# Performance work log

Measured on AMD Instinct MI355X. Metric: run time of the kernel, lower is better.

Reference implementation:

```python
import jax, jax.numpy as jnp
import numpy as np

B, C, H, W, CI, COUT = 4, 256, 48, 48, 128, 1024


def conv1x1(x, w, b):
    # 1x1 conv: x (b,c,h,w), w (o,c), b (o,)
    return jnp.einsum('bchw,oc->bohw', x, w) + b[None, :, None, None]


def setup_inputs() -> dict:
    key = jax.random.key(0)
    ks = jax.random.split(key, 24)
    s = 0.05
    d = {
        'x': jax.random.normal(ks[0], (B, C, H, W), jnp.float32),
        'x1': jax.random.normal(ks[1], (B, C, H, W), jnp.float32),
        'x2': jax.random.normal(ks[2], (B, C, H, W), jnp.float32),
        'x_in': jax.random.normal(ks[3], (B, COUT, H, W), jnp.float32),
        'g_w': jax.random.normal(ks[4], (CI, C), jnp.float32) * s,
        'g_b': jnp.zeros((CI,), jnp.float32),
        'th_w': jax.random.normal(ks[5], (CI, C), jnp.float32) * s,
        'th_b': jnp.zeros((CI,), jnp.float32),
        'ph_w': jax.random.normal(ks[6], (CI, C), jnp.float32) * s,
        'ph_b': jnp.zeros((CI,), jnp.float32),
        'th1_w': jax.random.normal(ks[7], (CI, C), jnp.float32) * s,
        'th1_b': jnp.zeros((CI,), jnp.float32),
        'ph1_w': jax.random.normal(ks[8], (CI, C), jnp.float32) * s,
        'ph1_b': jnp.zeros((CI,), jnp.float32),
        'th2_w': jax.random.normal(ks[9], (CI, C), jnp.float32) * s,
        'th2_b': jnp.zeros((CI,), jnp.float32),
        'ph2_w': jax.random.normal(ks[10], (CI, C), jnp.float32) * s,
        'ph2_b': jnp.zeros((CI,), jnp.float32),
        'W_w': jax.random.normal(ks[11], (C, CI), jnp.float32) * s,
        'W_b': jnp.zeros((C,), jnp.float32),
        'W1_w': jax.random.normal(ks[12], (C, CI), jnp.float32) * s,
        'W1_b': jnp.zeros((C,), jnp.float32),
        'W2_w': jax.random.normal(ks[13], (C, CI), jnp.float32) * s,
        'W2_b': jnp.zeros((C,), jnp.float32),
        'dw_w': jax.random.normal(ks[14], (3 * C,), jnp.float32) * s,   # depthwise 1x1 = per-channel scale
        'dw_b': jnp.zeros((3 * C,), jnp.float32),
        'pw_w': jax.random.normal(ks[15], (COUT, 3 * C), jnp.float32) * s,
        'pw_b': jnp.zeros((COUT,), jnp.float32),
        'p': jnp.array([0.5], jnp.float32),
    }
    return d


def reference(x, x1, x2, x_in, g_w, g_b, th_w, th_b, ph_w, ph_b,
              th1_w, th1_b, ph1_w, ph1_b, th2_w, th2_b, ph2_w, ph2_b,
              W_w, W_b, W1_w, W1_b, W2_w, W2_b, dw_w, dw_b, pw_w, pw_b, p):
    b, _, h, w = x.shape
    n = h * w

    def flat(v):  # (b,c,h,w) -> (b,c,n)
        return v.reshape(b, v.shape[1], n)

    # g projections (same g applied to x, x1, x2); MaxPool(1) is identity
    g_x = flat(conv1x1(x, g_w, g_b)).transpose(0, 2, 1)    # (b,n,ci)
    g_x1 = flat(conv1x1(x1, g_w, g_b)).transpose(0, 2, 1)
    g_x2 = flat(conv1x1(x2, g_w, g_b)).transpose(0, 2, 1)

    # three attention branches (unscaled QK^T softmax)
    def attn(v, tw, tb, pw, pb):
        theta = flat(conv1x1(v, tw, tb)).transpose(0, 2, 1)  # (b,n,ci)
        phi = flat(conv1x1(v, pw, pb))                       # (b,ci,n)
        f = jnp.einsum('bnc,bcm->bnm', theta, phi)           # (b,n,n)
        return jax.nn.softmax(f, axis=-1)

    A = attn(x, th_w, th_b, ph_w, ph_b)
    A = A + attn(x1, th1_w, th1_b, ph1_w, ph1_b)
    A = A + attn(x2, th2_w, th2_b, ph2_w, ph2_b)  # sum of the three softmax maps

    def mix(gv, Ww, Wb, res):
        # y = (A0+A1+A2) @ g  ==  A0@g + A1@g + A2@g (distributive, exact)
        y = jnp.einsum('bnm,bmc->bnc', A, gv)                # (b,n,ci)
        y = y.transpose(0, 2, 1).reshape(b, CI, h, w)
        return conv1x1(y, Ww, Wb) + res

    z = mix(g_x, W_w, W_b, x)
    z1 = mix(g_x1, W1_w, W1_b, x1)
    z2 = mix(g_x2, W2_w, W2_b, x2)

    cat = jnp.concatenate([z, z1, z2], axis=1)               # (b,768,h,w)
    # DWConv: depthwise 1x1 (per-channel scale+bias) then pointwise 1x1
    dw = cat * dw_w[None, :, None, None] + dw_b[None, :, None, None]
    out = conv1x1(dw, pw_w, pw_b)                            # (b,1024,h,w)
    return x_in + p[0] * out
```

## Files before the change

kernel.cpp:

```cpp
#include <hip/hip_runtime.h>


typedef __attribute__((ext_vector_type(8))) short bf16x8;
typedef __attribute__((ext_vector_type(4))) float f32x4;
typedef unsigned short u16;
struct alignas(8) u16x4 { u16 x, y, z, w; };
struct alignas(16) u16x8 { u16 e[8]; };

constexpr int B_ = 4, C_ = 256, N_ = 2304, CI_ = 128;
constexpr long long NN_ = (long long)N_ * N_;

constexpr size_t B_WB = 0;
constexpr size_t B_WZ = 589824;
constexpr size_t B_PW = 786432;
constexpr size_t B_R1 = 2359296;
constexpr size_t B_R2 = 16515072;
constexpr size_t B_GP = 30670848;
constexpr size_t B_F  = 37748736;
constexpr size_t B_A  = 69599232;

__device__ __forceinline__ u16 f2bf(float f) {
  unsigned u = __float_as_uint(f);
  u += 0x7fff + ((u >> 16) & 1);
  return (u16)(u >> 16);
}
__device__ __forceinline__ u16 f2h(float f) {
  _Float16 h = (_Float16)f;
  return __builtin_bit_cast(u16, h);
}
__device__ __forceinline__ float h2f(u16 u) {
  return (float)__builtin_bit_cast(_Float16, u);
}

__device__ __forceinline__ void gload16(const void* g, void* l) {
  __builtin_amdgcn_global_load_lds((const __attribute__((address_space(1))) void*)g,
                                   (__attribute__((address_space(3))) void*)l,
                                   16, 0, 0);
}

template<int N> __device__ __forceinline__ void vwait() {
  asm volatile("s_waitcnt vmcnt(%0)" :: "i"(N) : "memory");
}
__device__ __forceinline__ void barrier_() {
  asm volatile("" ::: "memory");
  __builtin_amdgcn_s_barrier();
  asm volatile("" ::: "memory");
}

__device__ __forceinline__ int xcd_swz() {
  const int nwg = (int)gridDim.x, orig = (int)blockIdx.x;
  const int q = nwg >> 3, r = nwg & 7;
  const int xcd = orig & 7, pos = orig >> 3;
  return (xcd < r ? xcd * (q + 1) : r * (q + 1) + (xcd - r) * q) + pos;
}

__device__ __forceinline__ void stage32(const char* Ag, int ldaB,
                                        const char* Bg, int ldbB,
                                        char* As, char* Bs, int t) {
  #pragma unroll
  for (int c = 0; c < 2; ++c) {
    const int idx = (c * 256 + t) * 16;
    const int row = idx >> 6;
    const int gc = (idx & 63) ^ (((row >> 1) & 3) << 4);
    gload16(Ag + (size_t)row * ldaB + gc, As + idx);
    gload16(Bg + (size_t)row * ldbB + gc, Bs + idx);
  }
}

__device__ __forceinline__ void comp32(const char* As, const char* Bs,
                                       f32x4 (&acc)[4][4],
                                       int arow, int brow, int kb) {
  bf16x8 af[4], bfr[4];
  #pragma unroll
  for (int i = 0; i < 4; ++i) {
    af[i]  = *(const bf16x8*)(As + (arow + i * 16) * 64 + kb);
    bfr[i] = *(const bf16x8*)(Bs + (brow + i * 16) * 64 + kb);
  }
  __builtin_amdgcn_s_setprio(1);
  #pragma unroll
  for (int mf = 0; mf < 4; ++mf)
    #pragma unroll
    for (int nf = 0; nf < 4; ++nf)
      acc[mf][nf] = __builtin_amdgcn_mfma_f32_16x16x32_bf16(
          af[mf], bfr[nf], acc[mf][nf], 0, 0, 0);
  __builtin_amdgcn_s_setprio(0);
}

__device__ __forceinline__ void gemm256c(const char* Ab, int ldaB,
                                         const char* Bb, int ldbB,
                                         int kIters, f32x4 (&acc)[4][4],
                                         char* lds) {
  const int t = (int)threadIdx.x, l = t & 63, w = t >> 6;
  const int arow = (w >> 1) * 64 + (l & 15);
  const int brow = (w & 1) * 64 + (l & 15);
  const int kb = ((l >> 4) * 16) ^ ((((l & 15) >> 1) & 3) << 4);
  char* A0 = lds;          char* B0 = lds + 8192;
  char* A1 = lds + 16384;  char* B1 = lds + 24576;
  char* A2 = lds + 32768;  char* B2 = lds + 40960;
  stage32(Ab,      ldaB, Bb,      ldbB, A0, B0, t);
  stage32(Ab + 64, ldaB, Bb + 64, ldbB, A1, B1, t);
  for (int kt = 0; kt < kIters - 2; ++kt) {
    stage32(Ab + (size_t)(kt + 2) * 64, ldaB,
            Bb + (size_t)(kt + 2) * 64, ldbB, A2, B2, t);
    vwait<8>();
    barrier_();
    comp32(A0, B0, acc, arow, brow, kb);
    barrier_();
    char* ta = A0; A0 = A1; A1 = A2; A2 = ta;
    char* tb = B0; B0 = B1; B1 = B2; B2 = tb;
  }
  vwait<4>();
  barrier_();
  comp32(A0, B0, acc, arow, brow, kb);
  vwait<0>();
  barrier_();
  comp32(A1, B1, acc, arow, brow, kb);
}

#define EPI_SETUP \
  const int el = (int)threadIdx.x & 63, ew = (int)threadIdx.x >> 6; \
  const int rb = (ew >> 1) * 64 + ((el >> 4) << 2); \
  const int cb = (ew & 1) * 64 + (el & 15);

struct CvtW { const float* s[13]; };
__global__ __launch_bounds__(256) void k_cvtw(CvtW cw, u16* dst) {
  const int seg = blockIdx.y;
  const int i = (blockIdx.x * 256 + threadIdx.x) * 4;
  const int sz = (seg == 12) ? 786432 : 32768;
  if (i >= sz) return;
  size_t off = (seg < 9) ? (size_t)seg * 32768
             : (seg < 12) ? 294912 + (size_t)(seg - 9) * 32768
                          : 393216;
  f32x4 v = *(const f32x4*)(cw.s[seg] + i);
  u16x4 o; o.x = f2bf(v[0]); o.y = f2bf(v[1]); o.z = f2bf(v[2]); o.w = f2bf(v[3]);
  *(u16x4*)(dst + off + i) = o;
}

__global__ __launch_bounds__(256) void k_cvtx(const float* x0, const float* x1,
                                              const float* x2, u16* XT) {
  __shared__ float tile[64][65];
  const int t = threadIdx.x;
  const int q0 = blockIdx.x * 64, c0 = blockIdx.y * 64;
  const int vb = blockIdx.z, v = vb >> 2, b = vb & 3;
  const float* src = (v == 0 ? x0 : v == 1 ? x1 : x2) + ((size_t)b * C_ + c0) * N_ + q0;
  #pragma unroll
  for (int i = 0; i < 4; ++i) {
    int idx = t + i * 256;
    int r = idx >> 4, q4 = (idx & 15) * 4;
    f32x4 val = *(const f32x4*)(src + (size_t)r * N_ + q4);
    tile[r][q4 + 0] = val[0]; tile[r][q4 + 1] = val[1];
    tile[r][q4 + 2] = val[2]; tile[r][q4 + 3] = val[3];
  }
  __syncthreads();
  u16* dst = XT + ((size_t)vb * N_ + q0) * 256 + c0;
  const int q = t >> 2, cp = (t & 3) * 16;
  u16 tmp[16];
  #pragma unroll
  for (int jj = 0; jj < 16; ++jj) tmp[jj] = f2bf(tile[cp + jj][q]);
  #pragma unroll
  for (int s4 = 0; s4 < 4; ++s4) {
    u16x4 o; o.x = tmp[s4 * 4]; o.y = tmp[s4 * 4 + 1];
    o.z = tmp[s4 * 4 + 2]; o.w = tmp[s4 * 4 + 3];
    *(u16x4*)(dst + (size_t)q * 256 + cp + s4 * 4) = o;
  }
}

struct ProjA { const float* bias[9]; };
__global__ __launch_bounds__(256) void k_proj(const u16* WB, const u16* XT,
                                              u16* TH, u16* PH, u16* GP, ProjA pa) {
  __shared__ char lds[49152];
  const int col0 = blockIdx.x * 128;
  const int p = blockIdx.z >> 2, b = blockIdx.z & 3;
  const int v = p / 3, pt = p % 3;
  const char* Ab = (const char*)(WB + (size_t)p * 32768);
  const char* Bb = (const char*)(XT + ((size_t)(v * 4 + b) * N_ + col0) * 256);
  f32x4 acc[4][4] = {};
  gemm256c(Ab, 512, Bb, 512, 8, acc, lds);
  EPI_SETUP;
  const float* bias = pa.bias[p];
  if (pt == 0) {
    u16* dst = GP + (size_t)(v * 4 + b) * CI_ * N_;
    #pragma unroll
    for (int mf = 0; mf < 4; ++mf) {
      const int row = rb + mf * 16;
      f32x4 bv = *(const f32x4*)(bias + row);
      #pragma unroll
      for (int nf = 0; nf < 4; ++nf) {
        const int col = col0 + cb + nf * 16;
        #pragma unroll
        for (int r = 0; r < 4; ++r)
          dst[(size_t)(row + r) * N_ + col] = f2bf(acc[mf][nf][r] + bv[r]);
      }
    }
  } else {
    u16* dst = (pt == 1 ? TH : PH) + (size_t)(v * 4 + b) * N_ * CI_;
    #pragma unroll
    for (int mf = 0; mf < 4; ++mf) {
      const int row = rb + mf * 16;
      f32x4 bv = *(const f32x4*)(bias + row);
      #pragma unroll
      for (int nf = 0; nf < 4; ++nf) {
        const int col = col0 + cb + nf * 16;
        u16x4 o;
        o.x = f2bf(acc[mf][nf][0] + bv[0]); o.y = f2bf(acc[mf][nf][1] + bv[1]);
        o.z = f2bf(acc[mf][nf][2] + bv[2]); o.w = f2bf(acc[mf][nf][3] + bv[3]);
        *(u16x4*)(dst + (size_t)col * CI_ + row) = o;
      }
    }
  }
}

__global__ __launch_bounds__(256) void k_score(const u16* TH, const u16* PH,
                                               u16* F, int b) {
  __shared__ char lds[49152];
  const int col0 = blockIdx.x * 128;
  const int row0 = blockIdx.y * 128;
  const int br = blockIdx.z;
  const char* Ab = (const char*)(TH + ((size_t)(br * 4 + b) * N_ + row0) * CI_);
  const char* Bb = (const char*)(PH + ((size_t)(br * 4 + b) * N_ + col0) * CI_);
  f32x4 acc[4][4] = {};
  gemm256c(Ab, 256, Bb, 256, 4, acc, lds);
  EPI_SETUP;
  const int t = (int)threadIdx.x;
  __syncthreads();
  u16* tl = (u16*)lds;
  #pragma unroll
  for (int mf = 0; mf < 4; ++mf)
    #pragma unroll
    for (int nf = 0; nf < 4; ++nf)
      #pragma unroll
      for (int r = 0; r < 4; ++r)
        tl[(rb + mf * 16 + r) * 136 + cb + nf * 16] = f2h(acc[mf][nf][r]);
  __syncthreads();
  u16* dst = F + (size_t)br * NN_;
  const int k8 = (t & 15) * 8;
  #pragma unroll
  for (int rr = 0; rr < 8; ++rr) {
    const int q = (t >> 4) + rr * 16;
    *(u16x8*)(dst + (size_t)(row0 + q) * N_ + col0 + k8) =
        *(const u16x8*)(tl + q * 136 + k8);
  }
}

__device__ __forceinline__ float blk_sum(float v, float* red) {
  #pragma unroll
  for (int o = 32; o; o >>= 1) v += __shfl_xor(v, o);
  int w = threadIdx.x >> 6;
  __syncthreads();
  if ((threadIdx.x & 63) == 0) red[w] = v;
  __syncthreads();
  return red[0] + red[1] + red[2] + red[3];
}

__global__ __launch_bounds__(256) void k_softsum(const u16* F, u16* Abf, int b) {
  __shared__ float red[4];
  const int q = blockIdx.x, t = threadIdx.x;
  const bool ext = (t < 32);
  float outv[16] = {};
  #pragma unroll
  for (int i = 0; i < 3; ++i) {
    const u16* base = F + (size_t)i * NN_ + (size_t)q * N_;
    float e[16];
    u16x8 a = *(const u16x8*)(base + t * 8);
    #pragma unroll
    for (int jj = 0; jj < 8; ++jj) e[jj] = __expf(h2f(a.e[jj]));
    if (ext) {
      u16x8 c = *(const u16x8*)(base + 2048 + t * 8);
      #pragma unroll
      for (int jj = 0; jj < 8; ++jj) e[8 + jj] = __expf(h2f(c.e[jj]));
    } else {
      #pragma unroll
      for (int jj = 0; jj < 8; ++jj) e[8 + jj] = 0.f;
    }
    float ssum = 0.f;
    #pragma unroll
    for (int s = 0; s < 16; ++s) ssum += e[s];
    ssum = blk_sum(ssum, red);
    const float inv = 1.f / ssum;
    #pragma unroll
    for (int s = 0; s < 16; ++s) outv[s] += e[s] * inv;
  }
  u16* dst = Abf + ((size_t)b * N_ + q) * N_;
  u16x8 o;
  #pragma unroll
  for (int jj = 0; jj < 8; ++jj) o.e[jj] = f2bf(outv[jj]);
  *(u16x8*)(dst + t * 8) = o;
  if (ext) {
    #pragma unroll
    for (int jj = 0; jj < 8; ++jj) o.e[jj] = f2bf(outv[8 + jj]);
    *(u16x8*)(dst + 2048 + t * 8) = o;
  }
}

__global__ __launch_bounds__(256) void k_pv(const u16* Abf, const u16* GP,
                                            float* P) {
  __shared__ char lds[49152];
  const int lid = xcd_swz();
  const int j = lid % 3;
  const int row0 = ((lid / 3) % 18) * 128;
  const int z = lid / 54;
  const int b = z >> 1, s = z & 1;
  const char* Ab = (const char*)(Abf + ((size_t)b * N_ + row0) * N_ + s * 1152);
  const char* Bb = (const char*)(GP + (size_t)(j * 4 + b) * CI_ * N_ + s * 1152);
  f32x4 acc[4][4] = {};
  gemm256c(Ab, 4608, Bb, 4608, 36, acc, lds);
  EPI_SETUP;
  const int t = (int)threadIdx.x;
  float* dst = P + ((size_t)(s * 4 + b) * N_) * 384;
  float* tl = (float*)lds;
  const int jc4 = (t & 15) * 4;
  #pragma unroll
  for (int p = 0; p < 2; ++p) {
    __syncthreads();
    if ((ew & 1) == p) {
      #pragma unroll
      for (int mf = 0; mf < 4; ++mf)
        #pragma unroll
        for (int nf = 0; nf < 4; ++nf)
          #pragma unroll
          for (int r = 0; r < 4; ++r)
            tl[(rb + mf * 16 + r) * 68 + (el & 15) + nf * 16] = acc[mf][nf][r];
    }
    __syncthreads();
    #pragma unroll
    for (int rr = 0; rr < 8; ++rr) {
      const int q = (t >> 4) + rr * 16;
      *(f32x4*)(dst + (size_t)(row0 + q) * 384 + j * 128 + p * 64 + jc4) =
          *(const f32x4*)(tl + q * 68 + jc4);
    }
  }
}

__global__ __launch_bounds__(256) void k_pvred(const float* P, u16* Y) {
  const size_t i4 = (size_t)blockIdx.x * 256 + threadIdx.x;
  constexpr size_t HALF = (size_t)4 * N_ * 384;
  f32x4 a = *(const f32x4*)(P + i4 * 4);
  f32x4 c = *(const f32x4*)(P + HALF + i4 * 4);
  u16x4 o; o.x = f2bf(a[0] + c[0]); o.y = f2bf(a[1] + c[1]);
  o.z = f2bf(a[2] + c[2]); o.w = f2bf(a[3] + c[3]);
  *(u16x4*)(Y + i4 * 4) = o;
}

struct ZA { const float* x[3]; const float* wzb[3]; const float* dww; const float* dwb; };
__global__ __launch_bounds__(256) void k_zcat(const u16* WZ, const u16* Y,
                                              u16* DW, ZA za) {
  __shared__ char lds[49152];
  const int col0 = blockIdx.x * 128;
  const int row0 = blockIdx.y * 128;
  const int j = blockIdx.z >> 2, b = blockIdx.z & 3;
  const char* Ab = (const char*)(WZ + (size_t)j * 32768 + (size_t)row0 * CI_);
  const char* Bb = (const char*)(Y + ((size_t)b * N_ + col0) * 384 + j * CI_);
  f32x4 acc[4][4] = {};
  gemm256c(Ab, 256, Bb, 768, 4, acc, lds);
  EPI_SETUP;
  const float* xj = za.x[j];
  #pragma unroll
  for (int mf = 0; mf < 4; ++mf) {
    const int cl = row0 + rb + mf * 16;
    const int cg = j * 256 + cl;
    f32x4 wb = *(const f32x4*)(za.wzb[j] + cl);
    f32x4 sc = *(const f32x4*)(za.dww + cg);
    f32x4 sb = *(const f32x4*)(za.dwb + cg);
    #pragma unroll
    for (int nf = 0; nf < 4; ++nf) {
      const int qg = col0 + cb + nf * 16;
      u16x4 o;
      o.x = f2bf((acc[mf][nf][0] + wb[0] + xj[((size_t)b * C_ + cl + 0) * N_ + qg]) * sc[0] + sb[0]);
      o.y = f2bf((acc[mf][nf][1] + wb[1] + xj[((size_t)b * C_ + cl + 1) * N_ + qg]) * sc[1] + sb[1]);
      o.z = f2bf((acc[mf][nf][2] + wb[2] + xj[((size_t)b * C_ + cl + 2) * N_ + qg]) * sc[2] + sb[2]);
      o.w = f2bf((acc[mf][nf][3] + wb[3] + xj[((size_t)b * C_ + cl + 3) * N_ + qg]) * sc[3] + sb[3]);
      *(u16x4*)(DW + ((size_t)b * N_ + qg) * 768 + cg) = o;
    }
  }
}

__global__ __launch_bounds__(256) void k_final(const u16* PWb, const u16* DW,
                                               const float* pwb, const float* xin,
                                               const float* pp, float* out) {
  __shared__ char lds[49152];
  const int lid = xcd_swz();
  const int row0 = (lid % 18) * 128;
  const int col0 = ((lid / 18) % 8) * 128;
  const int b = lid / 144;
  const char* Ab = (const char*)(DW + ((size_t)b * N_ + row0) * 768);
  const char* Bb = (const char*)(PWb + (size_t)col0 * 768);
  EPI_SETUP;
  const int t = (int)threadIdx.x;
  const float pscale = pp[0];
  const int q4 = (t & 31) * 4;
  const int ob = (t >> 5) * 8;
  f32x4 xv[2][8];
  #pragma unroll
  for (int p = 0; p < 2; ++p)
    #pragma unroll
    for (int rr = 0; rr < 8; ++rr)
      xv[p][rr] = *(const f32x4*)(
          xin + ((size_t)b * 1024 + col0 + p * 64 + ob + rr) * N_ + row0 + q4);
  f32x4 acc[4][4] = {};
  gemm256c(Ab, 1536, Bb, 1536, 24, acc, lds);
  float* tl = (float*)lds;
  #pragma unroll
  for (int p = 0; p < 2; ++p) {
    __syncthreads();
    if ((ew & 1) == p) {
      #pragma unroll
      for (int mf = 0; mf < 4; ++mf)
        #pragma unroll
        for (int nf = 0; nf < 4; ++nf)
          #pragma unroll
          for (int r = 0; r < 4; ++r)
            tl[((el & 15) + nf * 16) * 132 + rb + mf * 16 + r] = acc[mf][nf][r];
    }
    __syncthreads();
    #pragma unroll
    for (int rr = 0; rr < 8; ++rr) {
      const int og = col0 + p * 64 + ob + rr;
      const float bb = pwb[og];
      f32x4 a4 = *(const f32x4*)(tl + (ob + rr) * 132 + q4);
      f32x4 o4;
      #pragma unroll
      for (int r = 0; r < 4; ++r)
        o4[r] = xv[p][rr][r] + pscale * (a4[r] + bb);
      *(f32x4*)(out + ((size_t)b * 1024 + og) * N_ + row0 + q4) = o4;
    }
  }
}

extern "C" void kernel_launch(void* const* d_in, const int* in_sizes, int n_in,
                              void* d_out, int out_size, void* d_ws, size_t ws_size,
                              hipStream_t stream) {
  const float* x0  = (const float*)d_in[0];
  const float* x1  = (const float*)d_in[1];
  const float* x2  = (const float*)d_in[2];
  const float* xin = (const float*)d_in[3];
  const float* g_w = (const float*)d_in[4];
  const float* g_b = (const float*)d_in[5];
  const float* thw[3] = {(const float*)d_in[6],  (const float*)d_in[10], (const float*)d_in[14]};
  const float* thb[3] = {(const float*)d_in[7],  (const float*)d_in[11], (const float*)d_in[15]};
  const float* phw[3] = {(const float*)d_in[8],  (const float*)d_in[12], (const float*)d_in[16]};
  const float* phb[3] = {(const float*)d_in[9],  (const float*)d_in[13], (const float*)d_in[17]};
  const float* Wm[3]  = {(const float*)d_in[18], (const float*)d_in[20], (const float*)d_in[22]};
  const float* Wmb[3] = {(const float*)d_in[19], (const float*)d_in[21], (const float*)d_in[23]};
  const float* dww = (const float*)d_in[24];
  const float* dwb = (const float*)d_in[25];
  const float* pww = (const float*)d_in[26];
  const float* pwb = (const float*)d_in[27];
  const float* pp  = (const float*)d_in[28];

  char* wsb = (char*)d_ws;
  u16*   WB  = (u16*)(wsb + B_WB);
  u16*   WZ  = (u16*)(wsb + B_WZ);
  u16*   PW  = (u16*)(wsb + B_PW);
  u16*   XT  = (u16*)(wsb + B_R1);
  u16*   Y   = (u16*)(wsb + B_R1);
  u16*   TH  = (u16*)(wsb + B_R2);
  u16*   PH  = TH + (size_t)3 * B_ * N_ * CI_;
  u16*   DW  = (u16*)(wsb + B_R2);
  u16*   GP  = (u16*)(wsb + B_GP);
  u16*   Fh  = (u16*)(wsb + B_F);
  float* Pp  = (float*)(wsb + B_F);
  u16*   Abf = (u16*)(wsb + B_A);

  CvtW cw;
  cw.s[0] = g_w; cw.s[1] = thw[0]; cw.s[2] = phw[0];
  cw.s[3] = g_w; cw.s[4] = thw[1]; cw.s[5] = phw[1];
  cw.s[6] = g_w; cw.s[7] = thw[2]; cw.s[8] = phw[2];
  cw.s[9] = Wm[0]; cw.s[10] = Wm[1]; cw.s[11] = Wm[2];
  cw.s[12] = pww;

  ProjA pa;
  pa.bias[0] = g_b; pa.bias[1] = thb[0]; pa.bias[2] = phb[0];
  pa.bias[3] = g_b; pa.bias[4] = thb[1]; pa.bias[5] = phb[1];
  pa.bias[6] = g_b; pa.bias[7] = thb[2]; pa.bias[8] = phb[2];

  ZA za;
  za.x[0] = x0; za.x[1] = x1; za.x[2] = x2;
  za.wzb[0] = Wmb[0]; za.wzb[1] = Wmb[1]; za.wzb[2] = Wmb[2];
  za.dww = dww; za.dwb = dwb;

  k_cvtw<<<dim3(768, 13), 256, 0, stream>>>(cw, WB);
  k_cvtx<<<dim3(36, 4, 12), 256, 0, stream>>>(x0, x1, x2, XT);
  k_proj<<<dim3(18, 1, 36), 256, 0, stream>>>(WB, XT, TH, PH, GP, pa);
  for (int b = 0; b < B_; ++b) {
    k_score  <<<dim3(18, 18, 3), 256, 0, stream>>>(TH, PH, Fh, b);
    k_softsum<<<dim3(N_),        256, 0, stream>>>(Fh, Abf, b);
  }
  k_pv   <<<dim3(432),  256, 0, stream>>>(Abf, GP, Pp);
  k_pvred<<<dim3(3456), 256, 0, stream>>>(Pp, Y);
  k_zcat <<<dim3(18, 2, 12), 256, 0, stream>>>(WZ, Y, DW, za);
  k_final<<<dim3(576),  256, 0, stream>>>(PW, DW, pwb, xin, pp, (float*)d_out);
}
```

Baseline: 210.7 us.

## Deepen GEMM LDS ring to four stages and drop per-iteration trailing barrier

The shared GEMM main loop moves from a rotating three-buffer scheme to a four-slot LDS ring. There are now three tiles in flight, and the next tile is issued after the MFMA block. The fourth slot means the write target is the tile consumed in the previous iteration, so the second barrier per k-step can be removed. The cost is that every GEMM kernel now reserves 64KB of LDS instead of 48KB. That may reduce how many blocks fit per CU.

```diff
diff --git a/kernel.cpp b/kernel.cpp
--- a/kernel.cpp
+++ b/kernel.cpp
@@ -94,27 +94,36 @@
   const int arow = (w >> 1) * 64 + (l & 15);
   const int brow = (w & 1) * 64 + (l & 15);
   const int kb = ((l >> 4) * 16) ^ ((((l & 15) >> 1) & 3) << 4);
-  char* A0 = lds;          char* B0 = lds + 8192;
-  char* A1 = lds + 16384;  char* B1 = lds + 24576;
-  char* A2 = lds + 32768;  char* B2 = lds + 40960;
-  stage32(Ab,      ldaB, Bb,      ldbB, A0, B0, t);
-  stage32(Ab + 64, ldaB, Bb + 64, ldbB, A1, B1, t);
-  for (int kt = 0; kt < kIters - 2; ++kt) {
-    stage32(Ab + (size_t)(kt + 2) * 64, ldaB,
-            Bb + (size_t)(kt + 2) * 64, ldbB, A2, B2, t);
+  stage32(Ab,       ldaB, Bb,       ldbB, lds,         lds + 8192,  t);
+  stage32(Ab + 64,  ldaB, Bb + 64,  ldbB, lds + 16384, lds + 24576, t);
+  stage32(Ab + 128, ldaB, Bb + 128, ldbB, lds + 32768, lds + 40960, t);
+  for (int kt = 0; kt + 4 <= kIters; ++kt) {
+    char* slot = lds + ((kt & 3) * 16384);
+    char* nslot = lds + (((kt + 3) & 3) * 16384);
     vwait<8>();
     barrier_();
-    comp32(A0, B0, acc, arow, brow, kb);
+    comp32(slot, slot + 8192, acc, arow, brow, kb);
+    stage32(Ab + (size_t)(kt + 3) * 64, ldaB,
+            Bb + (size_t)(kt + 3) * 64, ldbB, nslot, nslot + 8192, t);
+  }
+  {
+    char* slot = lds + (((kIters - 3) & 3) * 16384);
+    vwait<8>();
     barrier_();
-    char* ta = A0; A0 = A1; A1 = A2; A2 = ta;
-    char* tb = B0; B0 = B1; B1 = B2; B2 = tb;
-  }
-  vwait<4>();
-  barrier_();
-  comp32(A0, B0, acc, arow, brow, kb);
-  vwait<0>();
-  barrier_();
-  comp32(A1, B1, acc, arow, brow, kb);
+    comp32(slot, slot + 8192, acc, arow, brow, kb);
+  }
+  {
+    char* slot = lds + (((kIters - 2) & 3) * 16384);
+    vwait<4>();
+    barrier_();
+    comp32(slot, slot + 8192, acc, arow, brow, kb);
+  }
+  {
+    char* slot = lds + (((kIters - 1) & 3) * 16384);
+    vwait<0>();
+    barrier_();
+    comp32(slot, slot + 8192, acc, arow, brow, kb);
+  }
 }
 
 #define EPI_SETUP \
@@ -168,7 +177,7 @@
 struct ProjA { const float* bias[9]; };
 __global__ __launch_bounds__(256) void k_proj(const u16* WB, const u16* XT,
                                               u16* TH, u16* PH, u16* GP, ProjA pa) {
-  __shared__ char lds[49152];
+  __shared__ char lds[65536];
   const int col0 = blockIdx.x * 128;
   const int p = blockIdx.z >> 2, b = blockIdx.z & 3;
   const int v = p / 3, pt = p % 3;
@@ -212,7 +221,7 @@
 
 __global__ __launch_bounds__(256) void k_score(const u16* TH, const u16* PH,
                                                u16* F, int b) {
-  __shared__ char lds[49152];
+  __shared__ char lds[65536];
   const int col0 = blockIdx.x * 128;
   const int row0 = blockIdx.y * 128;
   const int br = blockIdx.z;
@@ -294,7 +303,7 @@
 
 __global__ __launch_bounds__(256) void k_pv(const u16* Abf, const u16* GP,
                                             float* P) {
-  __shared__ char lds[49152];
+  __shared__ char lds[65536];
   const int lid = xcd_swz();
   const int j = lid % 3;
   const int row0 = ((lid / 3) % 18) * 128;
@@ -344,7 +353,7 @@
 struct ZA { const float* x[3]; const float* wzb[3]; const float* dww; const float* dwb; };
 __global__ __launch_bounds__(256) void k_zcat(const u16* WZ, const u16* Y,
                                               u16* DW, ZA za) {
-  __shared__ char lds[49152];
+  __shared__ char lds[65536];
   const int col0 = blockIdx.x * 128;
   const int row0 = blockIdx.y * 128;
   const int j = blockIdx.z >> 2, b = blockIdx.z & 3;
@@ -377,7 +386,7 @@
 __global__ __launch_bounds__(256) void k_final(const u16* PWb, const u16* DW,
                                                const float* pwb, const float* xin,
                                                const float* pp, float* out) {
-  __shared__ char lds[49152];
+  __shared__ char lds[65536];
   const int lid = xcd_swz();
   const int row0 = (lid % 18) * 128;
   const int col0 = ((lid / 18) % 8) * 128;
```

Result: slower. 216.4 us (+2.7%).

## Enlarge final GEMM tile to 256x128 with 512 threads and 4-stage LDS pipeline

Applied to the files above, without the earlier changes.

The final pointwise-conv GEMM now uses 256-row tiles with 512-thread blocks, so the grid halves to 288 blocks. Its K loop becomes an inline 4-slot LDS ring with async loads issued three stages ahead, replacing the generic gemm256c helper. The aim is more reuse of the weight tile and better hiding of global-memory latency. The cost is twice the LDS per block, which limits occupancy, and fewer blocks than there are CUs on the device.

```diff
diff --git a/kernel.cpp b/kernel.cpp
--- a/kernel.cpp
+++ b/kernel.cpp
@@ -374,54 +374,95 @@
   }
 }
 
-__global__ __launch_bounds__(256) void k_final(const u16* PWb, const u16* DW,
+__global__ __launch_bounds__(512) void k_final(const u16* PWb, const u16* DW,
                                                const float* pwb, const float* xin,
                                                const float* pp, float* out) {
-  __shared__ char lds[49152];
+  __shared__ char lds[98304];
   const int lid = xcd_swz();
-  const int row0 = (lid % 18) * 128;
-  const int col0 = ((lid / 18) % 8) * 128;
-  const int b = lid / 144;
+  const int row0 = (lid % 9) * 256;
+  const int col0 = ((lid / 9) % 8) * 128;
+  const int b = lid / 72;
   const char* Ab = (const char*)(DW + ((size_t)b * N_ + row0) * 768);
   const char* Bb = (const char*)(PWb + (size_t)col0 * 768);
-  EPI_SETUP;
-  const int t = (int)threadIdx.x;
+  const int t = (int)threadIdx.x, l = t & 63, w = t >> 6;
+  const int arow = (w >> 1) * 64 + (l & 15);
+  const int brow = (w & 1) * 64 + (l & 15);
+  const int kb = ((l >> 4) * 16) ^ ((((l & 15) >> 1) & 3) << 4);
   const float pscale = pp[0];
-  const int q4 = (t & 31) * 4;
-  const int ob = (t >> 5) * 8;
+  const int xq = (t & 63) * 4;
+  const int xo = (t >> 6) * 8;
   f32x4 xv[2][8];
   #pragma unroll
   for (int p = 0; p < 2; ++p)
     #pragma unroll
     for (int rr = 0; rr < 8; ++rr)
       xv[p][rr] = *(const f32x4*)(
-          xin + ((size_t)b * 1024 + col0 + p * 64 + ob + rr) * N_ + row0 + q4);
+          xin + ((size_t)b * 1024 + col0 + p * 64 + xo + rr) * N_ + row0 + xq);
+
+  auto stageF = [&](int kt, char* slot) {
+    const char* Ag = Ab + (size_t)kt * 64;
+    const char* Bg = Bb + (size_t)kt * 64;
+    #pragma unroll
+    for (int c = 0; c < 2; ++c) {
+      const int idx = (c * 512 + t) * 16;
+      const int row = idx >> 6;
+      const int gc = (idx & 63) ^ (((row >> 1) & 3) << 4);
+      gload16(Ag + (size_t)row * 1536 + gc, slot + idx);
+    }
+    {
+      const int idx = t * 16;
+      const int row = idx >> 6;
+      const int gc = (idx & 63) ^ (((row >> 1) & 3) << 4);
+      gload16(Bg + (size_t)row * 1536 + gc, slot + 16384 + idx);
+    }
+  };
+
   f32x4 acc[4][4] = {};
-  gemm256c(Ab, 1536, Bb, 1536, 24, acc, lds);
+  stageF(0, lds);
+  stageF(1, lds + 24576);
+  stageF(2, lds + 49152);
+  constexpr int KI = 24;
+  for (int kt = 0; kt + 4 <= KI; ++kt) {
+    char* slot  = lds + (kt & 3) * 24576;
+    char* nslot = lds + ((kt + 3) & 3) * 24576;
+    vwait<6>();
+    barrier_();
+    comp32(slot, slot + 16384, acc, arow, brow, kb);
+    stageF(kt + 3, nslot);
+  }
+  { char* slot = lds + ((KI - 3) & 3) * 24576;
+    vwait<6>(); barrier_(); comp32(slot, slot + 16384, acc, arow, brow, kb); }
+  { char* slot = lds + ((KI - 2) & 3) * 24576;
+    vwait<3>(); barrier_(); comp32(slot, slot + 16384, acc, arow, brow, kb); }
+  { char* slot = lds + ((KI - 1) & 3) * 24576;
+    vwait<0>(); barrier_(); comp32(slot, slot + 16384, acc, arow, brow, kb); }
+
   float* tl = (float*)lds;
   #pragma unroll
   for (int p = 0; p < 2; ++p) {
     __syncthreads();
-    if ((ew & 1) == p) {
+    if ((w & 1) == p) {
       #pragma unroll
       for (int mf = 0; mf < 4; ++mf)
         #pragma unroll
         for (int nf = 0; nf < 4; ++nf)
           #pragma unroll
           for (int r = 0; r < 4; ++r)
-            tl[((el & 15) + nf * 16) * 132 + rb + mf * 16 + r] = acc[mf][nf][r];
+            tl[((l & 15) + nf * 16) * 260 + arow - (l & 15) + mf * 16 +
+               ((l >> 4) << 2) + r - ((w >> 1) * 64) + (w >> 1) * 64] =
+                acc[mf][nf][r];
     }
     __syncthreads();
     #pragma unroll
     for (int rr = 0; rr < 8; ++rr) {
-      const int og = col0 + p * 64 + ob + rr;
+      const int og = col0 + p * 64 + xo + rr;
       const float bb = pwb[og];
-      f32x4 a4 = *(const f32x4*)(tl + (ob + rr) * 132 + q4);
+      f32x4 a4 = *(const f32x4*)(tl + (xo + rr) * 260 + xq);
       f32x4 o4;
       #pragma unroll
       for (int r = 0; r < 4; ++r)
         o4[r] = xv[p][rr][r] + pscale * (a4[r] + bb);
-      *(f32x4*)(out + ((size_t)b * 1024 + og) * N_ + row0 + q4) = o4;
+      *(f32x4*)(out + ((size_t)b * 1024 + og) * N_ + row0 + xq) = o4;
     }
   }
 }
@@ -488,5 +529,5 @@
   k_pv   <<<dim3(432),  256, 0, stream>>>(Abf, GP, Pp);
   k_pvred<<<dim3(3456), 256, 0, stream>>>(Pp, Y);
   k_zcat <<<dim3(18, 2, 12), 256, 0, stream>>>(WZ, Y, DW, za);
-  k_final<<<dim3(576),  256, 0, stream>>>(PW, DW, pwb, xin, pp, (float*)d_out);
-}
+  k_final<<<dim3(288),  512, 0, stream>>>(PW, DW, pwb, xin, pp, (float*)d_out);
+}
```

New measurement: 215.5 us. 1.02x slower.
